# Kernel optimization log

Hardware: AMD Instinct MI355X
Metric: run time of the kernel (lower is better)

Reference implementation:

```python
import jax, jax.numpy as jnp
import numpy as np

DIM = 512
EDIM = 2 * DIM          # edim(=2) * dim
OUT_DIM = 512
KERNEL_SIZE = 4096
B, L = 4, 4096


def setup_inputs() -> dict:
    key = jax.random.key(0)
    k0, k1, k2, k3, k4 = jax.random.split(key, 5)
    embeddings = jax.random.normal(k0, (B, L, DIM), dtype=jnp.float32)
    logit_alpha = jax.random.uniform(k1, (EDIM,), minval=-3.0, maxval=3.0, dtype=jnp.float32)
    logit_delta = jax.random.uniform(k2, (EDIM,), minval=-3.0, maxval=3.0, dtype=jnp.float32)
    # xavier_uniform: U(-a, a), a = sqrt(6/(fan_in+fan_out))
    a_beta = float(np.sqrt(6.0 / (DIM + EDIM)))
    beta = jax.random.uniform(k3, (DIM, EDIM), minval=-a_beta, maxval=a_beta, dtype=jnp.float32)
    a_eta = float(np.sqrt(6.0 / (EDIM + OUT_DIM)))
    eta = jax.random.uniform(k4, (EDIM, OUT_DIM), minval=-a_eta, maxval=a_eta, dtype=jnp.float32)
    return {"embeddings": embeddings, "logit_alpha": logit_alpha,
            "logit_delta": logit_delta, "beta": beta, "eta": eta}


def reference(embeddings, logit_alpha, logit_delta, beta, eta):
    K = KERNEL_SIZE
    Lseq = embeddings.shape[1]
    # data-dependent EMA decay kernel: kernel[e, t] = p_e * q_e^t
    alpha = jax.nn.sigmoid(logit_alpha)[:, None]            # [E, 1]
    delta = jax.nn.sigmoid(logit_delta)[:, None]            # [E, 1]
    p = alpha
    q = 1.0 - alpha * delta
    len_range = jnp.arange(K, dtype=embeddings.dtype)[None, :]   # [1, K]
    kernel = p * jnp.exp(jnp.log(q) * len_range)            # [E, K]

    u = jnp.einsum('bld,de->ble', embeddings, beta)         # [B, L, E]
    u_T = jnp.swapaxes(u, -1, -2)                           # [B, E, L]

    # forward (causal) direction: flip kernel, full conv via FFT, slice at K-1
    kernel_f = jnp.flip(kernel, axis=-1)
    fft_dim = Lseq + K
    fft_dim = 1 << (fft_dim - 1).bit_length()               # next power of 2 (static)
    inp_fft = jnp.fft.rfft(u_T, n=fft_dim, axis=-1)
    ker_fft = jnp.fft.rfft(kernel_f, n=fft_dim, axis=-1)    # [E, fft_dim//2+1]
    out_full = jnp.fft.irfft(inp_fft * ker_fft, n=fft_dim, axis=-1)
    out_T = out_full[..., K - 1:K - 1 + Lseq].astype(embeddings.dtype)  # [B, E, L]

    out = jnp.swapaxes(out_T, -1, -2)                       # [B, L, E]
    return jnp.einsum('ble,eo->blo', out, eta)              # [B, L, out_dim]
```

## Files before the change

### kernel.cpp

```cpp
#include <hip/hip_runtime.h>
#include <hip/hip_bf16.h>

#define DIM      512
#define EDIM     1024
#define OUTD     512
#define BATCH    4
#define LSEQ     4096
#define MROWS    (BATCH * LSEQ)
#define NCHUNK   64
#define CHUNK    (LSEQ / NCHUNK)

typedef __attribute__((ext_vector_type(8))) __bf16 bf16x8;
typedef __attribute__((ext_vector_type(4))) float  f32x4;

static __device__ __forceinline__ ushort f2b(float f) {
    uint x = __float_as_uint(f);
    x += 0x7fff + ((x >> 16) & 1);
    return (ushort)(x >> 16);
}
static __device__ __forceinline__ float b2f(ushort u) {
    return __uint_as_float(((uint)u) << 16);
}
static __device__ __forceinline__ float sigmoidf(float x) {
    return 1.0f / (1.0f + expf(-x));
}

__global__ void prep_cvt_kernel(const float* __restrict__ emb,
                                ushort* __restrict__ a16,
                                const float* __restrict__ beta,
                                const float* __restrict__ eta,
                                const float* __restrict__ la,
                                const float* __restrict__ ld,
                                ushort* __restrict__ betaT,
                                ushort* __restrict__ etaT,
                                float* __restrict__ p,
                                float* __restrict__ q) {
    __shared__ float tf[32][33];
    int blk = blockIdx.x;
    if (blk < 8192) {
        int i = blk * 256 + threadIdx.x;
        float4 v = ((const float4*)emb)[i];
        ushort4 o;
        o.x = f2b(v.x); o.y = f2b(v.y); o.z = f2b(v.z); o.w = f2b(v.w);
        ((ushort4*)a16)[i] = o;
    } else if (blk < 8704) {
        int tile = blk - 8192;
        int tr = tile >> 5, tc = tile & 31;
        int r = threadIdx.x >> 3, c4 = (threadIdx.x & 7) * 4;
        float4 v = *(const float4*)(beta + (size_t)(tr * 32 + r) * EDIM + tc * 32 + c4);
        tf[r][c4 + 0] = v.x; tf[r][c4 + 1] = v.y;
        tf[r][c4 + 2] = v.z; tf[r][c4 + 3] = v.w;
        __syncthreads();
        ushort4 o;
        o.x = f2b(tf[c4 + 0][r]); o.y = f2b(tf[c4 + 1][r]);
        o.z = f2b(tf[c4 + 2][r]); o.w = f2b(tf[c4 + 3][r]);
        *(ushort4*)(betaT + (size_t)(tc * 32 + r) * DIM + tr * 32 + c4) = o;
    } else if (blk < 9216) {
        int tile = blk - 8704;
        int tr = tile >> 4, tc = tile & 15;
        int r = threadIdx.x >> 3, c4 = (threadIdx.x & 7) * 4;
        float4 v = *(const float4*)(eta + (size_t)(tr * 32 + r) * OUTD + tc * 32 + c4);
        tf[r][c4 + 0] = v.x; tf[r][c4 + 1] = v.y;
        tf[r][c4 + 2] = v.z; tf[r][c4 + 3] = v.w;
        __syncthreads();
        ushort4 o;
        o.x = f2b(tf[c4 + 0][r]); o.y = f2b(tf[c4 + 1][r]);
        o.z = f2b(tf[c4 + 2][r]); o.w = f2b(tf[c4 + 3][r]);
        *(ushort4*)(etaT + (size_t)(tc * 32 + r) * EDIM + tr * 32 + c4) = o;
    } else {
        #pragma unroll
        for (int j = 0; j < 4; ++j) {
            int e = threadIdx.x * 4 + j;
            float a = sigmoidf(la[e]);
            float d = sigmoidf(ld[e]);
            p[e] = a;
            q[e] = 1.0f - a * d;
        }
    }
}

#define MFMA_BF16 __builtin_amdgcn_mfma_f32_16x16x32_bf16

template <int KDIM, int BN, int NSHIFT, int OUT_BF16, int DO_AGG>
__global__ __launch_bounds__(512, 2) void gemmr4(const ushort* __restrict__ A,
                                                 const ushort* __restrict__ Bt,
                                                 void* __restrict__ Cv,
                                                 const float* __restrict__ qv,
                                                 float* __restrict__ aggp,
                                                 int N) {
    constexpr int NF   = BN / 64;
    constexpr int LB   = BN / 128;
    constexpr int TILE = 16384 + BN * 64;
    constexpr int NT   = KDIM / 32;

    extern __shared__ __align__(16) char smem[];
    const int tid  = threadIdx.x;
    const int lane = tid & 63;
    const int wid  = tid >> 6;
    const int wr   = wid >> 2;
    const int wc   = wid & 3;
    const int l15  = lane & 15;
    const int l4   = lane >> 4;

    const int nwg  = gridDim.x;
    const int flat = ((int)blockIdx.x & 7) * (nwg >> 3) + ((int)blockIdx.x >> 3);
    const int rowBase = (flat >> NSHIFT) << 8;
    const int colBase = (flat & ((1 << NSHIFT) - 1)) * BN;

    const int srT = tid >> 3;
    const int slT = (tid & 7) ^ (srT & 7);
    const int rowT = 2 * srT + (slT >> 2);
    const int kT   = (slT & 3) * 8;
    const ushort* gA0 = A  + (size_t)(rowBase + rowT) * KDIM + kT;
    const ushort* gA1 = gA0 + (size_t)128 * KDIM;
    const ushort* gB0 = Bt + (size_t)(colBase + rowT) * KDIM + kT;
    const ushort* gB1 = gB0 + (size_t)128 * KDIM;

    const int l7 = l15 >> 1;
    const int sx = ((((l15 & 1) * 4 + l4) ^ l7)) << 4;
    const int aBase = (wr * 64 + l7) * 128 + sx;
    const int bBase = 16384 + (wc * (BN / 8) + l7) * 128 + sx;

    f32x4 acc[8][NF] = {};
    bf16x8 af[8], bfr[NF];

    auto ISSUE = [&](int t) {
        const int boff = (t & 3) * TILE;
        const size_t ko = (size_t)t * 32;
        __builtin_amdgcn_global_load_lds(
            (const __attribute__((address_space(1))) void*)(gA0 + ko),
            (__attribute__((address_space(3))) void*)(smem + boff + tid * 16), 16, 0, 0);
        __builtin_amdgcn_global_load_lds(
            (const __attribute__((address_space(1))) void*)(gA1 + ko),
            (__attribute__((address_space(3))) void*)(smem + boff + 8192 + tid * 16), 16, 0, 0);
        __builtin_amdgcn_global_load_lds(
            (const __attribute__((address_space(1))) void*)(gB0 + ko),
            (__attribute__((address_space(3))) void*)(smem + boff + 16384 + tid * 16), 16, 0, 0);
        if (LB == 2)
            __builtin_amdgcn_global_load_lds(
                (const __attribute__((address_space(1))) void*)(gB1 + ko),
                (__attribute__((address_space(3))) void*)(smem + boff + 24576 + tid * 16), 16, 0, 0);
    };

    ISSUE(0); ISSUE(1); ISSUE(2);
    if (LB == 2) asm volatile("s_waitcnt vmcnt(8)" ::: "memory");
    else         asm volatile("s_waitcnt vmcnt(6)" ::: "memory");
    __builtin_amdgcn_s_barrier();

    for (int t = 0; t < NT; ++t) {
        if (t + 3 < NT) ISSUE(t + 3);
        const char* sm = smem + (t & 3) * TILE;
        #pragma unroll
        for (int m = 0; m < 8; ++m)
            af[m] = *(const bf16x8*)(sm + aBase + m * 1024);
        #pragma unroll
        for (int n = 0; n < NF; ++n)
            bfr[n] = *(const bf16x8*)(sm + bBase + n * 1024);
        __builtin_amdgcn_s_setprio(1);
        #pragma unroll
        for (int m = 0; m < 8; ++m)
            #pragma unroll
            for (int n = 0; n < NF; ++n)
                acc[m][n] = MFMA_BF16(af[m], bfr[n], acc[m][n], 0, 0, 0);
        __builtin_amdgcn_s_setprio(0);
        if (t < NT - 3) {
            if (LB == 2) asm volatile("s_waitcnt vmcnt(8)" ::: "memory");
            else         asm volatile("s_waitcnt vmcnt(6)" ::: "memory");
        } else if (t == NT - 3) {
            if (LB == 2) asm volatile("s_waitcnt vmcnt(4)" ::: "memory");
            else         asm volatile("s_waitcnt vmcnt(3)" ::: "memory");
        } else if (t == NT - 2) {
            asm volatile("s_waitcnt vmcnt(0)" ::: "memory");
        }
        if (t < NT - 1) __builtin_amdgcn_s_barrier();
    }

    #pragma unroll
    for (int m = 0; m < 8; ++m)
        #pragma unroll
        for (int n = 0; n < NF; ++n)
            #pragma unroll
            for (int r = 0; r < 4; ++r) {
                int row = rowBase + wr * 128 + m * 16 + l4 * 4 + r;
                int col = colBase + wc * (BN / 4) + n * 16 + l15;
                if (OUT_BF16)
                    ((ushort*)Cv)[(size_t)row * N + col] = f2b(acc[m][n][r]);
                else
                    ((float*)Cv)[(size_t)row * N + col] = acc[m][n][r];
            }

    if (DO_AGG) {
        const int bidx = rowBase >> 12;
        const int chunkBase = ((rowBase & 4095) >> 6) + wr * 2;
        #pragma unroll
        for (int h = 0; h < 2; ++h) {
            #pragma unroll
            for (int n = 0; n < NF; ++n) {
                int col = colBase + wc * (BN / 4) + n * 16 + l15;
                float qe = qv[col];
                float q2 = qe * qe, q4 = q2 * q2, q8 = q4 * q4, q16 = q8 * q8;
                float P = 0.0f;
                #pragma unroll
                for (int m = 3; m >= 0; --m) {
                    f32x4 a = acc[h * 4 + m][n];
                    float pm = ((a[3] * qe + a[2]) * qe + a[1]) * qe + a[0];
                    P = P * q16 + pm;
                }
                float ql4 = (l4 & 1 ? q4 : 1.0f) * (l4 & 2 ? q8 : 1.0f);
                P *= ql4;
                P += __shfl_xor(P, 16, 64);
                P += __shfl_xor(P, 32, 64);
                if (l4 == 0)
                    aggp[(((bidx << 6) | (chunkBase + h)) << 10) + col] = P;
            }
        }
    }
}

__global__ void scan_apply_kernel(ushort* __restrict__ u,
                                  const float* __restrict__ pv,
                                  const float* __restrict__ qv,
                                  const float* __restrict__ agg) {
    int t = blockIdx.x * blockDim.x + threadIdx.x;
    int e0 = (t & 255) * 4;
    int c  = (t >> 8) & 63;
    int b  = t >> 14;
    float4 qe4 = *(const float4*)(qv + e0);
    float4 pe4 = *(const float4*)(pv + e0);
    float qe[4] = {qe4.x, qe4.y, qe4.z, qe4.w};
    float pe[4] = {pe4.x, pe4.y, pe4.z, pe4.w};
    float qL[4], S[4], w[4];
    #pragma unroll
    for (int k = 0; k < 4; ++k) {
        float x = qe[k];
        #pragma unroll
        for (int s = 0; s < 6; ++s) x *= x;
        qL[k] = x; S[k] = 0.0f; w[k] = 1.0f;
    }
    for (int cp = c + 1; cp < NCHUNK; ++cp) {
        float4 a = *(const float4*)(agg + (((b << 6) | cp) << 10) + e0);
        S[0] += w[0] * a.x;  w[0] *= qL[0];
        S[1] += w[1] * a.y;  w[1] *= qL[1];
        S[2] += w[2] * a.z;  w[2] *= qL[2];
        S[3] += w[3] * a.w;  w[3] *= qL[3];
    }
    ushort* up = u + ((size_t)(b * LSEQ + c * CHUNK) << 10) + e0;
    #pragma unroll 4
    for (int j = CHUNK - 1; j >= 0; --j) {
        ushort4 uv = *(ushort4*)(up + (size_t)j * EDIM);
        ushort4 ov;
        S[0] = b2f(uv.x) + qe[0] * S[0];  ov.x = f2b(pe[0] * S[0]);
        S[1] = b2f(uv.y) + qe[1] * S[1];  ov.y = f2b(pe[1] * S[1]);
        S[2] = b2f(uv.z) + qe[2] * S[2];  ov.z = f2b(pe[2] * S[2]);
        S[3] = b2f(uv.w) + qe[3] * S[3];  ov.w = f2b(pe[3] * S[3]);
        *(ushort4*)(up + (size_t)j * EDIM) = ov;
    }
}

extern "C" void kernel_launch(void* const* d_in, const int* in_sizes, int n_in,
                              void* d_out, int out_size, void* d_ws, size_t ws_size,
                              hipStream_t stream) {
    const float* emb  = (const float*)d_in[0];
    const float* la   = (const float*)d_in[1];
    const float* ld   = (const float*)d_in[2];
    const float* beta = (const float*)d_in[3];
    const float* eta  = (const float*)d_in[4];

    char* ws = (char*)d_ws;
    ushort* a16   = (ushort*)(ws);
    ushort* betaT = (ushort*)(ws + 16777216);
    ushort* etaT  = (ushort*)(ws + 17825792);
    ushort* u     = (ushort*)(ws + 18874368);
    float*  p     = (float*) (ws + 52428800);
    float*  q     = (float*) (ws + 52432896);
    float*  agg   = (float*) (ws + 52436992);

    (void)hipFuncSetAttribute((const void*)gemmr4<512, 256, 2, 1, 1>,
                              hipFuncAttributeMaxDynamicSharedMemorySize, 131072);
    (void)hipFuncSetAttribute((const void*)gemmr4<1024, 128, 2, 0, 0>,
                              hipFuncAttributeMaxDynamicSharedMemorySize, 98304);

    prep_cvt_kernel<<<dim3(9217), dim3(256), 0, stream>>>(
        emb, a16, beta, eta, la, ld, betaT, etaT, p, q);

    gemmr4<512, 256, 2, 1, 1><<<dim3(256), dim3(512), 131072, stream>>>(
        a16, betaT, (void*)u, q, agg, EDIM);

    scan_apply_kernel<<<dim3(256), dim3(256), 0, stream>>>(u, p, q, agg);

    gemmr4<1024, 128, 2, 0, 0><<<dim3(256), dim3(512), 98304, stream>>>(
        u, etaT, d_out, nullptr, nullptr, OUTD);
}
```

Before: 81.97 us.

## Fuse fp32-to-bf16 embedding conversion into first GEMM's LDS load path

Removes the separate pass that converted the 32 MB fp32 embeddings to bf16 in workspace. A new dedicated first GEMM streams fp32 A tiles straight into LDS via global_load_lds with a triple-buffered pipeline, then converts to bf16 in registers with v_cvt_pk_bf16_f32 before the MFMAs. This saves writing and re-reading a 16 MB intermediate, at the cost of twice the A-tile bytes per K step, larger LDS use (147 KB), and extra conversion ALU work in the GEMM inner loop.

```diff
diff --git a/kernel.cpp b/kernel.cpp
--- a/kernel.cpp
+++ b/kernel.cpp
@@ -24,28 +24,27 @@
 static __device__ __forceinline__ float sigmoidf(float x) {
     return 1.0f / (1.0f + expf(-x));
 }
-
-__global__ void prep_cvt_kernel(const float* __restrict__ emb,
-                                ushort* __restrict__ a16,
-                                const float* __restrict__ beta,
-                                const float* __restrict__ eta,
-                                const float* __restrict__ la,
-                                const float* __restrict__ ld,
-                                ushort* __restrict__ betaT,
-                                ushort* __restrict__ etaT,
-                                float* __restrict__ p,
-                                float* __restrict__ q) {
+static __device__ __forceinline__ bf16x8 cvt8(float4 lo, float4 hi) {
+    int4 r;
+    asm("v_cvt_pk_bf16_f32 %0, %1, %2" : "=v"(r.x) : "v"(lo.x), "v"(lo.y));
+    asm("v_cvt_pk_bf16_f32 %0, %1, %2" : "=v"(r.y) : "v"(lo.z), "v"(lo.w));
+    asm("v_cvt_pk_bf16_f32 %0, %1, %2" : "=v"(r.z) : "v"(hi.x), "v"(hi.y));
+    asm("v_cvt_pk_bf16_f32 %0, %1, %2" : "=v"(r.w) : "v"(hi.z), "v"(hi.w));
+    return __builtin_bit_cast(bf16x8, r);
+}
+
+__global__ void prep_kernel(const float* __restrict__ beta,
+                            const float* __restrict__ eta,
+                            const float* __restrict__ la,
+                            const float* __restrict__ ld,
+                            ushort* __restrict__ betaT,
+                            ushort* __restrict__ etaT,
+                            float* __restrict__ p,
+                            float* __restrict__ q) {
     __shared__ float tf[32][33];
     int blk = blockIdx.x;
-    if (blk < 8192) {
-        int i = blk * 256 + threadIdx.x;
-        float4 v = ((const float4*)emb)[i];
-        ushort4 o;
-        o.x = f2b(v.x); o.y = f2b(v.y); o.z = f2b(v.z); o.w = f2b(v.w);
-        ((ushort4*)a16)[i] = o;
-    } else if (blk < 8704) {
-        int tile = blk - 8192;
-        int tr = tile >> 5, tc = tile & 31;
+    if (blk < 512) {
+        int tr = blk >> 5, tc = blk & 31;
         int r = threadIdx.x >> 3, c4 = (threadIdx.x & 7) * 4;
         float4 v = *(const float4*)(beta + (size_t)(tr * 32 + r) * EDIM + tc * 32 + c4);
         tf[r][c4 + 0] = v.x; tf[r][c4 + 1] = v.y;
@@ -55,8 +54,8 @@
         o.x = f2b(tf[c4 + 0][r]); o.y = f2b(tf[c4 + 1][r]);
         o.z = f2b(tf[c4 + 2][r]); o.w = f2b(tf[c4 + 3][r]);
         *(ushort4*)(betaT + (size_t)(tc * 32 + r) * DIM + tr * 32 + c4) = o;
-    } else if (blk < 9216) {
-        int tile = blk - 8704;
+    } else if (blk < 1024) {
+        int tile = blk - 512;
         int tr = tile >> 4, tc = tile & 15;
         int r = threadIdx.x >> 3, c4 = (threadIdx.x & 7) * 4;
         float4 v = *(const float4*)(eta + (size_t)(tr * 32 + r) * OUTD + tc * 32 + c4);
@@ -80,13 +79,150 @@
 }
 
 #define MFMA_BF16 __builtin_amdgcn_mfma_f32_16x16x32_bf16
-
-template <int KDIM, int BN, int NSHIFT, int OUT_BF16, int DO_AGG>
+#define G1TILE 49152
+#define G1NT   16
+
+__global__ __launch_bounds__(512, 2) void gemm1_f32a(
+        const float* __restrict__ Af, const ushort* __restrict__ Bt,
+        ushort* __restrict__ Cv, const float* __restrict__ qv,
+        float* __restrict__ aggp) {
+    extern __shared__ __align__(16) char smem[];
+    const int tid  = threadIdx.x;
+    const int lane = tid & 63;
+    const int wid  = tid >> 6;
+    const int wr   = wid >> 2;
+    const int wc   = wid & 3;
+    const int l15  = lane & 15;
+    const int l4   = lane >> 4;
+
+    const int nwg  = gridDim.x;
+    const int flat = ((int)blockIdx.x & 7) * (nwg >> 3) + ((int)blockIdx.x >> 3);
+    const int rowBase = (flat >> 2) << 8;
+    const int colBase = (flat & 3) << 8;
+
+    const int ar[4] = { (0 * 512 + tid) >> 3, (1 * 512 + tid) >> 3,
+                        (2 * 512 + tid) >> 3, (3 * 512 + tid) >> 3 };
+    const int srT  = tid >> 3;
+    const int slT  = (tid & 7) ^ (srT & 7);
+    const int rowT = 2 * srT + (slT >> 2);
+    const int kT   = (slT & 3) * 8;
+
+    const float*  gA[4];
+    #pragma unroll
+    for (int r = 0; r < 4; ++r) {
+        int c  = r * 512 + tid;
+        int sl = (c & 7) ^ (ar[r] & 7);
+        gA[r] = Af + (size_t)(rowBase + ar[r]) * DIM + sl * 4;
+    }
+    const ushort* gB0 = Bt + (size_t)(colBase + rowT) * DIM + kT;
+    const ushort* gB1 = gB0 + (size_t)128 * DIM;
+
+    const int sA  = l15 & 7;
+    const int aB  = (wr * 128 + l15) * 128;
+    const int a0  = aB + (((l4 * 2)     ^ sA) << 4);
+    const int a1  = aB + (((l4 * 2 + 1) ^ sA) << 4);
+    const int l7  = l15 >> 1;
+    const int sx  = ((((l15 & 1) * 4 + l4) ^ l7)) << 4;
+    const int bB  = 32768 + (wc * 32 + l7) * 128 + sx;
+
+    f32x4 acc[8][4] = {};
+    bf16x8 af[8], bfr[4];
+
+    auto ISSUE = [&](int t, char* slot) {
+        const size_t ko = (size_t)t * 32;
+        #pragma unroll
+        for (int r = 0; r < 4; ++r)
+            __builtin_amdgcn_global_load_lds(
+                (const __attribute__((address_space(1))) void*)(gA[r] + ko),
+                (__attribute__((address_space(3))) void*)(slot + (r * 512 + tid) * 16),
+                16, 0, 0);
+        __builtin_amdgcn_global_load_lds(
+            (const __attribute__((address_space(1))) void*)(gB0 + ko),
+            (__attribute__((address_space(3))) void*)(slot + 32768 + tid * 16), 16, 0, 0);
+        __builtin_amdgcn_global_load_lds(
+            (const __attribute__((address_space(1))) void*)(gB1 + ko),
+            (__attribute__((address_space(3))) void*)(slot + 40960 + tid * 16), 16, 0, 0);
+    };
+
+    char* slot0 = smem;
+    char* slot1 = smem + G1TILE;
+    char* slot2 = smem + 2 * G1TILE;
+
+    ISSUE(0, slot0);
+    ISSUE(1, slot1);
+    asm volatile("s_waitcnt vmcnt(6)" ::: "memory");
+    __builtin_amdgcn_s_barrier();
+
+    for (int t = 0; t < G1NT; ++t) {
+        if (t + 2 < G1NT) ISSUE(t + 2, slot2);
+        const char* sm = slot0;
+        #pragma unroll
+        for (int n = 0; n < 4; ++n)
+            bfr[n] = *(const bf16x8*)(sm + bB + n * 1024);
+        #pragma unroll
+        for (int m = 0; m < 8; ++m) {
+            float4 lo = *(const float4*)(sm + a0 + m * 2048);
+            float4 hi = *(const float4*)(sm + a1 + m * 2048);
+            af[m] = cvt8(lo, hi);
+        }
+        __builtin_amdgcn_s_setprio(1);
+        #pragma unroll
+        for (int m = 0; m < 8; ++m)
+            #pragma unroll
+            for (int n = 0; n < 4; ++n)
+                acc[m][n] = MFMA_BF16(af[m], bfr[n], acc[m][n], 0, 0, 0);
+        __builtin_amdgcn_s_setprio(0);
+        if (t + 2 < G1NT)
+            asm volatile("s_waitcnt vmcnt(6)" ::: "memory");
+        else if (t + 1 < G1NT)
+            asm volatile("s_waitcnt vmcnt(0)" ::: "memory");
+        if (t + 1 < G1NT) __builtin_amdgcn_s_barrier();
+        char* tmp = slot0; slot0 = slot1; slot1 = slot2; slot2 = tmp;
+    }
+
+    #pragma unroll
+    for (int m = 0; m < 8; ++m)
+        #pragma unroll
+        for (int n = 0; n < 4; ++n)
+            #pragma unroll
+            for (int r = 0; r < 4; ++r) {
+                int row = rowBase + wr * 128 + m * 16 + l4 * 4 + r;
+                int col = colBase + wc * 64 + n * 16 + l15;
+                Cv[(size_t)row * EDIM + col] = f2b(acc[m][n][r]);
+            }
+
+    {
+        const int bidx = rowBase >> 12;
+        const int chunkBase = ((rowBase & 4095) >> 6) + wr * 2;
+        #pragma unroll
+        for (int h = 0; h < 2; ++h) {
+            #pragma unroll
+            for (int n = 0; n < 4; ++n) {
+                int col = colBase + wc * 64 + n * 16 + l15;
+                float qe = qv[col];
+                float q2 = qe * qe, q4 = q2 * q2, q8 = q4 * q4, q16 = q8 * q8;
+                float P = 0.0f;
+                #pragma unroll
+                for (int m = 3; m >= 0; --m) {
+                    f32x4 a = acc[h * 4 + m][n];
+                    float pm = ((a[3] * qe + a[2]) * qe + a[1]) * qe + a[0];
+                    P = P * q16 + pm;
+                }
+                float ql4 = (l4 & 1 ? q4 : 1.0f) * (l4 & 2 ? q8 : 1.0f);
+                P *= ql4;
+                P += __shfl_xor(P, 16, 64);
+                P += __shfl_xor(P, 32, 64);
+                if (l4 == 0)
+                    aggp[(((bidx << 6) | (chunkBase + h)) << 10) + col] = P;
+            }
+        }
+    }
+}
+
+template <int KDIM, int BN, int NSHIFT, int OUT_BF16>
 __global__ __launch_bounds__(512, 2) void gemmr4(const ushort* __restrict__ A,
                                                  const ushort* __restrict__ Bt,
                                                  void* __restrict__ Cv,
-                                                 const float* __restrict__ qv,
-                                                 float* __restrict__ aggp,
                                                  int N) {
     constexpr int NF   = BN / 64;
     constexpr int LB   = BN / 128;
@@ -188,33 +324,6 @@
                 else
                     ((float*)Cv)[(size_t)row * N + col] = acc[m][n][r];
             }
-
-    if (DO_AGG) {
-        const int bidx = rowBase >> 12;
-        const int chunkBase = ((rowBase & 4095) >> 6) + wr * 2;
-        #pragma unroll
-        for (int h = 0; h < 2; ++h) {
-            #pragma unroll
-            for (int n = 0; n < NF; ++n) {
-                int col = colBase + wc * (BN / 4) + n * 16 + l15;
-                float qe = qv[col];
-                float q2 = qe * qe, q4 = q2 * q2, q8 = q4 * q4, q16 = q8 * q8;
-                float P = 0.0f;
-                #pragma unroll
-                for (int m = 3; m >= 0; --m) {
-                    f32x4 a = acc[h * 4 + m][n];
-                    float pm = ((a[3] * qe + a[2]) * qe + a[1]) * qe + a[0];
-                    P = P * q16 + pm;
-                }
-                float ql4 = (l4 & 1 ? q4 : 1.0f) * (l4 & 2 ? q8 : 1.0f);
-                P *= ql4;
-                P += __shfl_xor(P, 16, 64);
-                P += __shfl_xor(P, 32, 64);
-                if (l4 == 0)
-                    aggp[(((bidx << 6) | (chunkBase + h)) << 10) + col] = P;
-            }
-        }
-    }
 }
 
 __global__ void scan_apply_kernel(ushort* __restrict__ u,
@@ -267,27 +376,25 @@
     const float* eta  = (const float*)d_in[4];
 
     char* ws = (char*)d_ws;
-    ushort* a16   = (ushort*)(ws);
-    ushort* betaT = (ushort*)(ws + 16777216);
-    ushort* etaT  = (ushort*)(ws + 17825792);
-    ushort* u     = (ushort*)(ws + 18874368);
-    float*  p     = (float*) (ws + 52428800);
-    float*  q     = (float*) (ws + 52432896);
-    float*  agg   = (float*) (ws + 52436992);
-
-    (void)hipFuncSetAttribute((const void*)gemmr4<512, 256, 2, 1, 1>,
-                              hipFuncAttributeMaxDynamicSharedMemorySize, 131072);
-    (void)hipFuncSetAttribute((const void*)gemmr4<1024, 128, 2, 0, 0>,
+    ushort* betaT = (ushort*)(ws);
+    ushort* etaT  = (ushort*)(ws + 1048576);
+    ushort* u     = (ushort*)(ws + 2097152);
+    float*  p     = (float*) (ws + 35651584);
+    float*  q     = (float*) (ws + 35655680);
+    float*  agg   = (float*) (ws + 35659776);
+
+    (void)hipFuncSetAttribute((const void*)gemm1_f32a,
+                              hipFuncAttributeMaxDynamicSharedMemorySize, 147456);
+    (void)hipFuncSetAttribute((const void*)gemmr4<1024, 128, 2, 0>,
                               hipFuncAttributeMaxDynamicSharedMemorySize, 98304);
 
-    prep_cvt_kernel<<<dim3(9217), dim3(256), 0, stream>>>(
-        emb, a16, beta, eta, la, ld, betaT, etaT, p, q);
-
-    gemmr4<512, 256, 2, 1, 1><<<dim3(256), dim3(512), 131072, stream>>>(
-        a16, betaT, (void*)u, q, agg, EDIM);
+    prep_kernel<<<dim3(1025), dim3(256), 0, stream>>>(beta, eta, la, ld,
+                                                      betaT, etaT, p, q);
+
+    gemm1_f32a<<<dim3(256), dim3(512), 147456, stream>>>(emb, betaT, u, q, agg);
 
     scan_apply_kernel<<<dim3(256), dim3(256), 0, stream>>>(u, p, q, agg);
 
-    gemmr4<1024, 128, 2, 0, 0><<<dim3(256), dim3(512), 98304, stream>>>(
-        u, etaT, d_out, nullptr, nullptr, OUTD);
-}
+    gemmr4<1024, 128, 2, 0><<<dim3(256), dim3(512), 98304, stream>>>(
+        u, etaT, d_out, OUTD);
+}
```

After: 86.03 us. +5.0%, slower.
